# Performance work log

Hardware: AMD Instinct MI355X
Metric: run time of the kernel (lower is better)

## Reference

```python
import jax, jax.numpy as jnp
import numpy as np

D_MODEL = 512
NUM_HEADS = 4
KEY_DIM = 512          # expand_k = 1.0
VALUE_DIM = 1024       # expand_v = 2.0
HEAD_QK = KEY_DIM // NUM_HEADS    # 128
HEAD_V = VALUE_DIM // NUM_HEADS   # 256
GATE_LOW_RANK = 16
GATE_LOGIT_NORMALIZER = 16
EPS = 1e-5
CHUNK = 64
B, HH, WW = 8, 56, 56
N = HH * WW


def rmsnorm(x, w, eps=EPS):
    return x * jax.lax.rsqrt(jnp.mean(x * x, axis=-1, keepdims=True) + eps) * w


def gla_chunk(q, k, v, gk, scale, chunk=CHUNK):
    """Chunked gated linear attention (causal, decay gate on key dim).
    q,k,gk: [B,H,N,dk], v: [B,H,N,dv]. Recurrence:
      S_t = diag(exp(gk_t)) S_{t-1} + k_t^T v_t ;  o_t = (q_t*scale) S_t
    """
    Bb, Hh, Nn, dk = q.shape
    dv = v.shape[-1]
    nc = Nn // chunk

    def rc(t):  # [B,H,N,d] -> [nc,B,H,chunk,d]
        return jnp.moveaxis(t.reshape(Bb, Hh, nc, chunk, t.shape[-1]), 2, 0)

    qs, ks, vs, gs = rc(q), rc(k), rc(v), rc(gk)
    b = jnp.cumsum(gs, axis=-2)  # inclusive intra-chunk log-decay
    mask = jnp.tril(jnp.ones((chunk, chunk), bool))

    def step(S, inp):
        q_, k_, v_, b_ = inp
        qe = q_ * jnp.exp(b_) * scale                      # [B,H,C,dk]
        A = jnp.einsum('bhtd,bhsd->bhts', qe, k_ * jnp.exp(-b_))
        A = jnp.where(mask, A, 0.0)                        # causal intra-chunk
        o = jnp.einsum('bhts,bhsv->bhtv', A, v_) \
            + jnp.einsum('bhtd,bhdv->bhtv', qe, S)         # inter-chunk
        btot = b_[..., -1:, :]                             # [B,H,1,dk]
        S = S * jnp.exp(btot[..., 0, :])[..., None] \
            + jnp.einsum('bhtd,bhtv->bhdv', k_ * jnp.exp(btot - b_), v_)
        return S, o

    S0 = jnp.zeros((Bb, Hh, dk, dv), q.dtype)
    _, os = jax.lax.scan(step, S0, (qs, ks, vs, b))
    return jnp.moveaxis(os, 0, 2).reshape(Bb, Hh, Nn, dv)


def setup_inputs() -> dict:
    key = jax.random.key(0)
    ks = jax.random.split(key, 9)
    s = 0.02
    return {
        'x': jax.random.normal(ks[0], (B, N, D_MODEL), jnp.float32),
        'conv_w': jax.random.normal(ks[1], (D_MODEL, 1, 3, 3), jnp.float32) * s,
        'qkv_w': jax.random.normal(ks[2], (2 * KEY_DIM + VALUE_DIM, D_MODEL), jnp.float32) * s,
        'gk_w1': jax.random.normal(ks[3], (GATE_LOW_RANK, D_MODEL), jnp.float32) * s,
        'gk_w2': jax.random.normal(ks[4], (2 * KEY_DIM, GATE_LOW_RANK), jnp.float32) * s,
        'gk_b2': jax.random.normal(ks[5], (2 * KEY_DIM,), jnp.float32) * s,
        'g_w': jax.random.normal(ks[6], (VALUE_DIM, D_MODEL), jnp.float32) * s,
        'g_b': jax.random.normal(ks[7], (VALUE_DIM,), jnp.float32) * s,
        'gnorm_w': jnp.ones((HEAD_V,), jnp.float32),
        'lnorm_w': jnp.ones((HEAD_V,), jnp.float32),
        'o_w': jax.random.normal(ks[8], (D_MODEL, VALUE_DIM), jnp.float32) * s,
        'hw_h': HH,
        'hw_w': WW,
    }


def reference(x, conv_w, qkv_w, gk_w1, gk_w2, gk_b2, g_w, g_b,
              gnorm_w, lnorm_w, o_w, hw_h, hw_w):
    Bb, Nn, C = x.shape
    # in_proj: depthwise 3x3 conv over spatial layout + SiLU
    x2d = x.reshape(Bb, hw_h, hw_w, C).transpose(0, 3, 1, 2)
    x2d = jax.lax.conv_general_dilated(
        x2d, conv_w, (1, 1), 'SAME',
        dimension_numbers=('NCHW', 'OIHW', 'NCHW'), feature_group_count=C)
    xs = jax.nn.silu(x2d).transpose(0, 2, 3, 1).reshape(Bb, Nn, C)

    qkv = xs @ qkv_w.T
    q, k, v = jnp.split(qkv, [KEY_DIM, 2 * KEY_DIM], axis=-1)

    def heads(t, d):  # [B,N,h*d] -> [B,h,N,d]
        return t.reshape(Bb, Nn, NUM_HEADS, d).transpose(0, 2, 1, 3)

    q, k, v = heads(q, HEAD_QK), heads(k, HEAD_QK), heads(v, HEAD_V)

    # low-rank gate projection, two groups (forward / backward scan)
    gk = (xs @ gk_w1.T) @ gk_w2.T + gk_b2
    gk = jax.nn.log_sigmoid(gk) / GATE_LOGIT_NORMALIZER
    gk_f, gk_b = jnp.split(gk, 2, axis=-1)
    gk_f, gk_b = heads(gk_f, HEAD_QK), heads(gk_b, HEAD_QK)

    scale = HEAD_QK ** -0.5
    o_f = gla_chunk(q, k, v, gk_f, scale)
    flip = lambda t: t[:, :, ::-1]
    o_b = flip(gla_chunk(flip(q), flip(k), flip(v), flip(gk_b), scale))

    o = rmsnorm(o_f, gnorm_w) + rmsnorm(o_b, lnorm_w)   # [B,h,N,dv]
    o = o.transpose(0, 2, 1, 3).reshape(Bb, Nn, VALUE_DIM)
    g = xs @ g_w.T + g_b
    o = jax.nn.silu(g) * o                              # swish output gate
    return o @ o_w.T
```

## Files before the change

### kernel.cpp

```cpp
#include <hip/hip_runtime.h>
#include <hip/hip_bf16.h>
#include <math.h>

#define NHEADS 4
#define DMODEL 512
#define HQK 128
#define HV 256
#define BBATCH 8
#define SH 56
#define SWW 56
#define SEQN (SH*SWW)
#define NTOK (BBATCH*SEQN)
#define CH2 32
#define NC2 (SEQN/CH2)


typedef __bf16 bf16x8 __attribute__((ext_vector_type(8)));
typedef float  f32x4  __attribute__((ext_vector_type(4)));

__device__ __forceinline__ float silu_f(float v){ return v / (1.f + __expf(-v)); }

__device__ __forceinline__ float b2f(unsigned short u){
  union { unsigned int i; float f; } c; c.i = ((unsigned int)u) << 16; return c.f;
}
__device__ __forceinline__ unsigned short f2b(float f){
  __bf16 h = (__bf16)f;
  unsigned short u; __builtin_memcpy(&u, &h, 2); return u;
}
__device__ __forceinline__ float h2f(unsigned short u){
  _Float16 h; __builtin_memcpy(&h, &u, 2); return (float)h;
}
__device__ __forceinline__ unsigned short f2h(float f){
  _Float16 h = (_Float16)f; unsigned short u; __builtin_memcpy(&u, &h, 2); return u;
}
__device__ __forceinline__ float lsig16(float z){
  float e = __expf(-fabsf(z));
  return (fminf(z, 0.f) - __logf(1.f + e)) * 0.0625f;
}
__device__ __forceinline__ void up8(uint4 v, unsigned short* o){
  o[0]=(unsigned short)v.x; o[1]=(unsigned short)(v.x>>16);
  o[2]=(unsigned short)v.y; o[3]=(unsigned short)(v.y>>16);
  o[4]=(unsigned short)v.z; o[5]=(unsigned short)(v.z>>16);
  o[6]=(unsigned short)v.w; o[7]=(unsigned short)(v.w>>16);
}
__device__ __forceinline__ uint4 pk8(const unsigned short* s){
  uint4 v;
  v.x = (unsigned)s[0] | ((unsigned)s[1]<<16);
  v.y = (unsigned)s[2] | ((unsigned)s[3]<<16);
  v.z = (unsigned)s[4] | ((unsigned)s[5]<<16);
  v.w = (unsigned)s[6] | ((unsigned)s[7]<<16);
  return v;
}

#define GLL16(gp, lp) __builtin_amdgcn_global_load_lds( \
    (const __attribute__((address_space(1))) unsigned int*)(gp), \
    (__attribute__((address_space(3))) unsigned int*)(lp), 16, 0, 0)

__global__ __launch_bounds__(256) void k_w2b(const float* __restrict__ w,
                                             unsigned short* __restrict__ o, int n){
  int i = (blockIdx.x*256 + threadIdx.x) << 2;
  if (i >= n) return;
  float4 v = *(const float4*)&w[i];
  ushort4 p;
  p.x = f2b(v.x); p.y = f2b(v.y); p.z = f2b(v.z); p.w = f2b(v.w);
  *(ushort4*)&o[i] = p;
}

__global__ __launch_bounds__(256) void k_wc(const float* __restrict__ w1,
                                            const float* __restrict__ w2,
                                            unsigned short* __restrict__ wc){
  int idx = blockIdx.x*256 + threadIdx.x;
  int n = idx >> 9, k = idx & 511;
  float acc = 0.f;
  #pragma unroll
  for (int r=0;r<16;++r) acc += w2[n*16+r]*w1[r*512+k];
  wc[idx] = f2b(acc);
}

__global__ __launch_bounds__(256) void k_conv_silu(const float* __restrict__ x,
                                                   const float* __restrict__ cw,
                                                   unsigned short* __restrict__ xs){
  int gid = blockIdx.x*256 + threadIdx.x;
  int c4  = (gid & 127) << 2;
  int tok = gid >> 7;
  int b = tok / SEQN, sp = tok % SEQN;
  int hh = sp / SWW, ww = sp % SWW;
  float a0=0.f,a1=0.f,a2=0.f,a3=0.f;
  #pragma unroll
  for (int dh=-1; dh<=1; ++dh){
    int h2 = hh+dh; if (h2<0||h2>=SH) continue;
    #pragma unroll
    for (int dw=-1; dw<=1; ++dw){
      int w2 = ww+dw; if (w2<0||w2>=SWW) continue;
      const float4 xv = *(const float4*)&x[((size_t)(b*SEQN + h2*SWW + w2))*DMODEL + c4];
      int tap = (dh+1)*3 + (dw+1);
      a0 += xv.x * cw[(c4+0)*9 + tap];
      a1 += xv.y * cw[(c4+1)*9 + tap];
      a2 += xv.z * cw[(c4+2)*9 + tap];
      a3 += xv.w * cw[(c4+3)*9 + tap];
    }
  }
  ushort4 o;
  o.x = f2b(silu_f(a0)); o.y = f2b(silu_f(a1)); o.z = f2b(silu_f(a2)); o.w = f2b(silu_f(a3));
  *(ushort4*)&xs[(size_t)tok*DMODEL + c4] = o;
}

template<int ACT, int CBF>
__global__ __launch_bounds__(256) void k_gemm_mfma(const unsigned short* __restrict__ A,
                                                   const unsigned short* __restrict__ W,
                                                   const float* __restrict__ bias,
                                                   void* __restrict__ Cv,
                                                   int M, int N, int K){
  __shared__ unsigned short sA[128*32];
  __shared__ unsigned short sB[128*32];
  const int tid  = threadIdx.x;
  const int wave = tid >> 6, lane = tid & 63;
  const int lm = lane & 15, quad = lane >> 4;
  const int wm = wave & 1, wn = wave >> 1;
  const int nwg = gridDim.x * gridDim.y;
  const int hb  = blockIdx.y * gridDim.x + blockIdx.x;
  const int fb  = (hb & 7) * (nwg >> 3) + (hb >> 3);
  const int m0 = (fb / gridDim.x) * 128, n0 = (fb % gridDim.x) * 128;

  const int r0 = tid >> 2,  c0 = (tid & 3) << 3;
  const int f1 = tid + 256;
  const int r1 = f1 >> 2,   c1 = (f1 & 3) << 3;

  f32x4 acc[4][4] = {};

  for (int kt = 0; kt < K; kt += 32){
    GLL16(&A[(size_t)(m0 + r0)*K + kt + c0], &sA[(size_t)tid*8]);
    GLL16(&A[(size_t)(m0 + r1)*K + kt + c1], &sA[(size_t)f1*8]);
    GLL16(&W[(size_t)(n0 + r0)*K + kt + c0], &sB[(size_t)tid*8]);
    GLL16(&W[(size_t)(n0 + r1)*K + kt + c1], &sB[(size_t)f1*8]);
    __syncthreads();
    bf16x8 af[4], bf[4];
    #pragma unroll
    for (int i=0;i<4;++i) af[i] = *(const bf16x8*)&sA[(wm*64 + i*16 + lm)*32 + quad*8];
    #pragma unroll
    for (int j=0;j<4;++j) bf[j] = *(const bf16x8*)&sB[(wn*64 + j*16 + lm)*32 + quad*8];
    #pragma unroll
    for (int i=0;i<4;++i)
      #pragma unroll
      for (int j=0;j<4;++j)
        acc[i][j] = __builtin_amdgcn_mfma_f32_16x16x32_bf16(af[i], bf[j], acc[i][j], 0, 0, 0);
    __syncthreads();
  }

  #pragma unroll
  for (int i=0;i<4;++i){
    #pragma unroll
    for (int r=0;r<4;++r){
      size_t m = (size_t)(m0 + wm*64 + i*16 + quad*4 + r);
      #pragma unroll
      for (int j=0;j<4;++j){
        int n = n0 + wn*64 + j*16 + lm;
        float v = acc[i][j][r];
        if (bias) v += bias[n];
        if (ACT==1) v = silu_f(v);
        if (CBF) ((unsigned short*)Cv)[m*(size_t)N + n] = f2b(v);
        else     ((float*)Cv)[m*(size_t)N + n] = v;
      }
    }
  }
}

__global__ __launch_bounds__(256) void k_prep(unsigned short* __restrict__ qkv,
                                              const unsigned short* __restrict__ z,
                                              unsigned short* __restrict__ dbuf,
                                              unsigned short* __restrict__ ebF,
                                              unsigned short* __restrict__ ebB){
  const int blk = blockIdx.x;
  const int bb = blk / NC2, cB = blk % NC2;
  const int j  = threadIdx.x << 1;
  const int cb = j & 0x180;
  const int sl = j & 127;
  const int d1 = ((sl & 7) << 4) | (sl >> 3);
  const int d2 = d1 + 16;
  const size_t base = (size_t)bb*SEQN + cB*CH2;
  const float sc = 0.08838834764831845f;
  float bf0[CH2], bf1[CH2];
  float r0 = 0.f, r1 = 0.f;
  #pragma unroll
  for (int t=0;t<CH2;++t){
    size_t tok = base + t;
    float z0 = b2f(z[tok*1024 + cb + d1]);
    float z1 = b2f(z[tok*1024 + cb + d2]);
    r0 += lsig16(z0);
    r1 += lsig16(z1);
    bf0[t] = r0; bf1[t] = r1;
    float qv1 = b2f(qkv[tok*2048 + cb + d1]);
    float qv2 = b2f(qkv[tok*2048 + cb + d2]);
    float kv1 = b2f(qkv[tok*2048 + 512 + cb + d1]);
    float kv2 = b2f(qkv[tok*2048 + 512 + cb + d2]);
    float e0 = __expf(r0),  e1 = __expf(r1);
    float n0 = __expf(-r0), n1 = __expf(-r1);
    unsigned qo = (unsigned)f2b(qv1*e0*sc) | ((unsigned)f2b(qv2*e1*sc) << 16);
    unsigned ko = (unsigned)f2b(kv1*n0)    | ((unsigned)f2b(kv2*n1) << 16);
    __syncthreads();
    *(unsigned*)&qkv[tok*2048 + j] = qo;
    *(unsigned*)&qkv[tok*2048 + 512 + j] = ko;
  }
  const int hh = j >> 7;
  {
    int ef = ((bb*NHEADS + hh)*NC2 + cB)*HQK;
    ebF[ef + d1] = f2h(__expf(bf0[CH2-1]));
    ebF[ef + d2] = f2h(__expf(bf1[CH2-1]));
  }
  r0 = 0.f; r1 = 0.f;
  #pragma unroll
  for (int t=CH2-1;t>=0;--t){
    size_t tok = base + t;
    float z0 = b2f(z[tok*1024 + 512 + cb + d1]);
    float z1 = b2f(z[tok*1024 + 512 + cb + d2]);
    r0 += lsig16(z0);
    r1 += lsig16(z1);
    float dd0 = r0 - bf0[t], dd1 = r1 - bf1[t];
    *(unsigned*)&dbuf[tok*512 + j] = (unsigned)f2h(__expf(dd0))
                                   | ((unsigned)f2h(__expf(dd1)) << 16);
  }
  {
    int eb = ((bb*NHEADS + hh)*NC2 + (NC2-1-cB))*HQK;
    ebB[eb + d1] = f2h(__expf(r0));
    ebB[eb + d2] = f2h(__expf(r1));
  }
}

#define SKET_STORE(sKeT_, kb_, o8_, ts_) \
  _Pragma("unroll") \
  for (int u=0;u<8;++u){ \
    (sKeT_)[(u*16 + 2*(o8_)    )*40 + (ts_)] = (kb_)[u]; \
    (sKeT_)[(u*16 + 2*(o8_) + 1)*40 + (ts_)] = (kb_)[u+8]; \
  }

__global__ __launch_bounds__(256,3) void k_gla_state(const unsigned short* __restrict__ qkvb,
                                                     const unsigned short* __restrict__ dbuf,
                                                     const unsigned short* __restrict__ ebFt,
                                                     const unsigned short* __restrict__ ebBt,
                                                     float* __restrict__ dSseg){
  __shared__ __align__(16) unsigned short sKeT[2][128*40];
  __shared__ __align__(16) unsigned short sVT[2][128*40];
  __shared__ float sEb[2][128];

  const int tid = threadIdx.x;
  const int bx = blockIdx.x;
  const int combo = bx & 127, seg = bx >> 7;
  const int vp = combo & 1, dir = (combo>>1)&1, hh = (combo>>2)&3, bb = (combo>>4)&7;

  const int w = tid >> 6, lane = tid & 63;
  const int quad = lane >> 4, lm = lane & 15;
  const int ts = tid >> 3, o8 = tid & 7, d16 = o8 << 4;
  const int tl = tid & 31, vg = tid >> 5;

  const int kcol = 512 + hh*HQK, vcol = 1024 + hh*HV + vp*128;
  const int dcol = hh*HQK;
  const unsigned short* ebT = dir ? ebBt : ebFt;
  const int ebBase = (bb*NHEADS + hh)*NC2*HQK;
  const int c0 = (seg==0)?0:(seg==1)?13:(seg==2)?25:(seg==3)?37:(seg==4)?50:62;
  const int c1 = (seg==0)?13:(seg==1)?25:(seg==2)?37:(seg==3)?50:(seg==4)?62:74;

#define STSTAGE(c_, bi_) { \
    int p_ = (c_)*CH2 + ts; \
    int n_ = dir ? (SEQN-1-p_) : p_; \
    size_t tok_ = (size_t)bb*SEQN + n_; \
    uint4 k0_ = *(const uint4*)&qkvb[tok_*2048 + kcol + d16]; \
    uint4 k1_ = *(const uint4*)&qkvb[tok_*2048 + kcol + d16 + 8]; \
    unsigned short kb_[16]; \
    up8(k0_, kb_); up8(k1_, kb_+8); \
    if (dir){ \
      uint4 dd0_ = *(const uint4*)&dbuf[tok_*512 + dcol + d16]; \
      uint4 dd1_ = *(const uint4*)&dbuf[tok_*512 + dcol + d16 + 8]; \
      unsigned short eh_[16]; \
      up8(dd0_, eh_); up8(dd1_, eh_+8); \
      _Pragma("unroll") \
      for (int u=0;u<16;++u) \
        kb_[u] = f2b(b2f(kb_[u]) * __builtin_amdgcn_rcpf(h2f(eh_[u]))); \
    } \
    SKET_STORE(sKeT[bi_], kb_, o8, ts); \
    int pv_ = (c_)*CH2 + tl; \
    int nv_ = dir ? (SEQN-1-pv_) : pv_; \
    size_t tokv_ = (size_t)bb*SEQN + nv_; \
    uint4 uv0_ = *(const uint4*)&qkvb[tokv_*2048 + vcol + vg*8]; \
    uint4 uv1_ = *(const uint4*)&qkvb[tokv_*2048 + vcol + 64 + vg*8]; \
    unsigned short su_[8]; \
    up8(uv0_, su_); \
    _Pragma("unroll") \
    for (int u=0;u<8;++u) sVT[bi_][(vg*8+u)*40 + tl] = su_[u]; \
    up8(uv1_, su_); \
    _Pragma("unroll") \
    for (int u=0;u<8;++u) sVT[bi_][(64+vg*8+u)*40 + tl] = su_[u]; \
    if (tid < 128) sEb[bi_][tid] = h2f(ebT[ebBase + (c_)*HQK + tid]); \
  }

  f32x4 Sreg[2][8];
  #pragma unroll
  for (int vh=0; vh<2; ++vh)
    #pragma unroll
    for (int i=0;i<8;++i)
      #pragma unroll
      for (int r=0;r<4;++r) Sreg[vh][i][r] = 0.f;

  STSTAGE(c0, 0);
  __syncthreads();
  for (int c = c0; c < c1; ++c){
    const int cur = (c - c0) & 1;
    if (c + 1 < c1) STSTAGE(c+1, cur^1);
    bf16x8 vta0 = *(const bf16x8*)&sVT[cur][(w*16+lm)*40 + quad*8];
    bf16x8 vta1 = *(const bf16x8*)&sVT[cur][(64 + w*16+lm)*40 + quad*8];
    #pragma unroll
    for (int dt=0; dt<8; ++dt){
      bf16x8 kt = *(const bf16x8*)&sKeT[cur][(dt*16+lm)*40 + quad*8];
      float eb = sEb[cur][dt*16 + lm];
      Sreg[0][dt] = __builtin_amdgcn_mfma_f32_16x16x32_bf16(vta0, kt, Sreg[0][dt], 0, 0, 0);
      Sreg[1][dt] = __builtin_amdgcn_mfma_f32_16x16x32_bf16(vta1, kt, Sreg[1][dt], 0, 0, 0);
      #pragma unroll
      for (int r=0;r<4;++r){ Sreg[0][dt][r] *= eb; Sreg[1][dt][r] *= eb; }
    }
    __syncthreads();
  }
#undef STSTAGE

  #pragma unroll
  for (int vh=0; vh<2; ++vh){
    const int combo_s = (vp*2+vh) | (dir<<2) | (hh<<3) | (bb<<5);
    const size_t sbase = ((size_t)seg*256 + combo_s) * 8192;
    #pragma unroll
    for (int dt=0; dt<8; ++dt){
      #pragma unroll
      for (int r=0;r<4;++r)
        dSseg[sbase + (size_t)(w*16 + quad*4 + r)*128 + dt*16 + lm] = Sreg[vh][dt][r];
    }
  }
}

__global__ __launch_bounds__(256) void k_gla_comb(const float* __restrict__ dSseg,
                                                  float* __restrict__ dSf,
                                                  const unsigned short* __restrict__ ebFt,
                                                  const unsigned short* __restrict__ ebBt){
  const int combo = blockIdx.x;
  const int dir = (combo>>2)&1, hh = (combo>>3)&3, bb = (combo>>5)&7;
  const unsigned short* ebT = dir ? ebBt : ebFt;
  const int ebBase = (bb*NHEADS + hh)*NC2*HQK;
  const int t = threadIdx.x;
  const int d0 = (t << 2) & 127;
  float D1[4]={1,1,1,1}, D2[4]={1,1,1,1}, D3[4]={1,1,1,1}, D4[4]={1,1,1,1}, D5[4]={1,1,1,1};
  for (int c=13; c<25; ++c){
    ushort4 ev = *(const ushort4*)&ebT[ebBase + c*HQK + d0];
    D1[0]*=h2f(ev.x); D1[1]*=h2f(ev.y); D1[2]*=h2f(ev.z); D1[3]*=h2f(ev.w);
  }
  for (int c=25; c<37; ++c){
    ushort4 ev = *(const ushort4*)&ebT[ebBase + c*HQK + d0];
    D2[0]*=h2f(ev.x); D2[1]*=h2f(ev.y); D2[2]*=h2f(ev.z); D2[3]*=h2f(ev.w);
  }
  for (int c=37; c<50; ++c){
    ushort4 ev = *(const ushort4*)&ebT[ebBase + c*HQK + d0];
    D3[0]*=h2f(ev.x); D3[1]*=h2f(ev.y); D3[2]*=h2f(ev.z); D3[3]*=h2f(ev.w);
  }
  for (int c=50; c<62; ++c){
    ushort4 ev = *(const ushort4*)&ebT[ebBase + c*HQK + d0];
    D4[0]*=h2f(ev.x); D4[1]*=h2f(ev.y); D4[2]*=h2f(ev.z); D4[3]*=h2f(ev.w);
  }
  for (int c=62; c<74; ++c){
    ushort4 ev = *(const ushort4*)&ebT[ebBase + c*HQK + d0];
    D5[0]*=h2f(ev.x); D5[1]*=h2f(ev.y); D5[2]*=h2f(ev.z); D5[3]*=h2f(ev.w);
  }
  const size_t bA = (size_t)combo*8192;
  const size_t SEG = (size_t)256*8192;
  #pragma unroll
  for (int r=0;r<8;++r){
    int idx = r*1024 + (t<<2);
    float4 a0 = *(const float4*)&dSseg[bA + idx];
    float4 a1 = *(const float4*)&dSseg[bA + SEG + idx];
    float4 a2 = *(const float4*)&dSseg[bA + 2*SEG + idx];
    float4 a3 = *(const float4*)&dSseg[bA + 3*SEG + idx];
    float4 a4 = *(const float4*)&dSseg[bA + 4*SEG + idx];
    float4 a5 = *(const float4*)&dSseg[bA + 5*SEG + idx];
    float4 s25, s50, s74;
    s25.x = D1[0]*a0.x + a1.x; s25.y = D1[1]*a0.y + a1.y;
    s25.z = D1[2]*a0.z + a1.z; s25.w = D1[3]*a0.w + a1.w;
    s50.x = D3[0]*(D2[0]*s25.x + a2.x) + a3.x;
    s50.y = D3[1]*(D2[1]*s25.y + a2.y) + a3.y;
    s50.z = D3[2]*(D2[2]*s25.z + a2.z) + a3.z;
    s50.w = D3[3]*(D2[3]*s25.w + a2.w) + a3.w;
    s74.x = D5[0]*(D4[0]*s50.x + a4.x) + a5.x;
    s74.y = D5[1]*(D4[1]*s50.y + a4.y) + a5.y;
    s74.z = D5[2]*(D4[2]*s50.z + a4.z) + a5.z;
    s74.w = D5[3]*(D4[3]*s50.w + a4.w) + a5.w;
    *(float4*)&dSf[bA + idx] = s25;
    *(float4*)&dSf[SEG + bA + idx] = s50;
    *(float4*)&dSf[2*SEG + bA + idx] = s74;
  }
}

__global__ __launch_bounds__(256,2) void k_gla3(const unsigned short* __restrict__ qkvb,
                                                const unsigned short* __restrict__ dbuf,
                                                const unsigned short* __restrict__ ebFt,
                                                const unsigned short* __restrict__ ebBt,
                                                unsigned short* __restrict__ og,
                                                const float* __restrict__ dSf){
  __shared__ __align__(16) unsigned short sQe[32*136];
  __shared__ __align__(16) unsigned short sKe[32*136];
  __shared__ __align__(16) unsigned short sKeT[128*40];
  __shared__ __align__(16) unsigned short sVT[128*40];
  __shared__ __align__(16) unsigned short sST[128*136];
  __shared__ __align__(16) unsigned short sP[32*40];
  __shared__ float sEb[128];

  const int tid = threadIdx.x;
  const int bx = blockIdx.x;
  const int combo = bx & 127, seg = bx >> 7;
  const int vp = combo & 1, dir = (combo>>1)&1, hh = (combo>>2)&3, bb = (combo>>4)&7;

  const int w = tid >> 6, lane = tid & 63;
  const int quad = lane >> 4, lm = lane & 15;
  const int mt = w >> 1, nt = w & 1;
  const int ts = tid >> 3, o8 = tid & 7, d16 = o8 << 4;
  const int tl = tid & 31, vg = tid >> 5;

  const int qcol = hh*HQK, kcol = 512 + hh*HQK, vcol = 1024 + hh*HV + vp*128;
  const int dcol = hh*HQK;
  const unsigned short* ebT = dir ? ebBt : ebFt;
  const int ebBase = (bb*NHEADS + hh)*NC2*HQK;
  const size_t ogBase = ((size_t)((dir*BBATCH + bb)*NHEADS + hh)) * SEQN * HV;

  f32x4 Sreg[2][8];
  #pragma unroll
  for (int vh=0; vh<2; ++vh)
    #pragma unroll
    for (int i=0;i<8;++i)
      #pragma unroll
      for (int r=0;r<4;++r) Sreg[vh][i][r] = 0.f;
  if (seg){
    #pragma unroll
    for (int vh=0; vh<2; ++vh){
      const int combo_s = (vp*2+vh) | (dir<<2) | (hh<<3) | (bb<<5);
      const size_t sbase = ((size_t)(seg-1)*256 + combo_s) * 8192;
      #pragma unroll
      for (int dt=0; dt<8; ++dt){
        #pragma unroll
        for (int r=0;r<4;++r){
          float sv = dSf[sbase + (size_t)(w*16 + quad*4 + r)*128 + dt*16 + lm];
          Sreg[vh][dt][r] = sv;
          sST[(vh*64 + w*16 + quad*4 + r)*136 + lm*8 + dt] = f2b(sv);
        }
      }
    }
  } else {
    for (int i = tid; i < 128*136; i += 256) sST[i] = 0;
  }
  __syncthreads();

  const int cBeg = (seg==0)?0:(seg==1)?25:(seg==2)?50:74;
  const int cEnd = (seg==0)?25:(seg==1)?50:(seg==2)?74:98;

  for (int c = cBeg; c < cEnd; ++c){
    {
      int p = c*CH2 + ts;
      int n = dir ? (SEQN-1-p) : p;
      size_t tok = (size_t)bb*SEQN + n;
      uint4 q0 = *(const uint4*)&qkvb[tok*2048 + qcol + d16];
      uint4 q1 = *(const uint4*)&qkvb[tok*2048 + qcol + d16 + 8];
      uint4 k0 = *(const uint4*)&qkvb[tok*2048 + kcol + d16];
      uint4 k1 = *(const uint4*)&qkvb[tok*2048 + kcol + d16 + 8];
      unsigned short kb[16];
      up8(k0, kb); up8(k1, kb+8);
      if (dir){
        uint4 dd0 = *(const uint4*)&dbuf[tok*512 + dcol + d16];
        uint4 dd1 = *(const uint4*)&dbuf[tok*512 + dcol + d16 + 8];
        unsigned short eh[16], qb[16];
        up8(dd0, eh); up8(dd1, eh+8);
        up8(q0, qb);  up8(q1, qb+8);
        #pragma unroll
        for (int u=0;u<16;++u){
          float e  = h2f(eh[u]);
          float ei = __builtin_amdgcn_rcpf(e);
          qb[u] = f2b(b2f(qb[u]) * e);
          kb[u] = f2b(b2f(kb[u]) * ei);
        }
        q0 = pk8(qb); q1 = pk8(qb+8);
        k0 = pk8(kb); k1 = pk8(kb+8);
      }
      *(uint4*)&sQe[ts*136 + d16]     = q0;
      *(uint4*)&sQe[ts*136 + d16 + 8] = q1;
      *(uint4*)&sKe[ts*136 + d16]     = k0;
      *(uint4*)&sKe[ts*136 + d16 + 8] = k1;
      SKET_STORE(sKeT, kb, o8, ts);
      int pv = c*CH2 + tl;
      int nv = dir ? (SEQN-1-pv) : pv;
      size_t tokv = (size_t)bb*SEQN + nv;
      uint4 uv0 = *(const uint4*)&qkvb[tokv*2048 + vcol + vg*8];
      uint4 uv1 = *(const uint4*)&qkvb[tokv*2048 + vcol + 64 + vg*8];
      unsigned short su[8];
      up8(uv0, su);
      #pragma unroll
      for (int u=0;u<8;++u) sVT[(vg*8+u)*40 + tl] = su[u];
      up8(uv1, su);
      #pragma unroll
      for (int u=0;u<8;++u) sVT[(64+vg*8+u)*40 + tl] = su[u];
    }
    if (tid < 128) sEb[tid] = h2f(ebT[ebBase + c*HQK + tid]);
    __syncthreads();
    bf16x8 qf[2][4];
    #pragma unroll
    for (int tt=0; tt<2; ++tt){
      #pragma unroll
      for (int ks=0; ks<4; ++ks)
        qf[tt][ks] = *(const bf16x8*)&sQe[(tt*16+lm)*136 + ks*32 + quad*8];
    }
    f32x4 a1;
    #pragma unroll
    for (int r=0;r<4;++r) a1[r] = 0.f;
    #pragma unroll
    for (int ks=0; ks<4; ++ks){
      bf16x8 kfr = *(const bf16x8*)&sKe[(nt*16+lm)*136 + ks*32 + quad*8];
      a1 = __builtin_amdgcn_mfma_f32_16x16x32_bf16(qf[mt][ks], kfr, a1, 0, 0, 0);
    }
    f32x4 ot[2][2];
    #pragma unroll
    for (int vh=0; vh<2; ++vh)
      #pragma unroll
      for (int tt=0; tt<2; ++tt)
        #pragma unroll
        for (int r=0;r<4;++r) ot[vh][tt][r] = 0.f;
    #pragma unroll
    for (int ks=0; ks<4; ++ks){
      #pragma unroll
      for (int vh=0; vh<2; ++vh){
        bf16x8 stf = *(const bf16x8*)&sST[(vh*64 + w*16+lm)*136 + ks*32 + quad*8];
        #pragma unroll
        for (int tt=0; tt<2; ++tt)
          ot[vh][tt] = __builtin_amdgcn_mfma_f32_16x16x32_bf16(stf, qf[tt][ks], ot[vh][tt], 0, 0, 0);
      }
    }
    #pragma unroll
    for (int r=0;r<4;++r){
      int t = mt*16 + quad*4 + r, s = nt*16 + lm;
      sP[t*40 + s] = f2b((s <= t) ? a1[r] : 0.f);
    }
    __syncthreads();
    bf16x8 vta[2];
    vta[0] = *(const bf16x8*)&sVT[(w*16+lm)*40 + quad*8];
    vta[1] = *(const bf16x8*)&sVT[(64 + w*16+lm)*40 + quad*8];
    #pragma unroll
    for (int dt=0; dt<8; ++dt){
      bf16x8 kt = *(const bf16x8*)&sKeT[(dt*16+lm)*40 + quad*8];
      float eb = sEb[dt*16 + lm];
      #pragma unroll
      for (int vh=0; vh<2; ++vh){
        Sreg[vh][dt] = __builtin_amdgcn_mfma_f32_16x16x32_bf16(vta[vh], kt, Sreg[vh][dt], 0, 0, 0);
        #pragma unroll
        for (int r=0;r<4;++r) Sreg[vh][dt][r] *= eb;
      }
    }
    #pragma unroll
    for (int vh=0; vh<2; ++vh){
      #pragma unroll
      for (int r=0;r<4;++r){
        uint4 pkv;
        pkv.x = (unsigned)f2b(Sreg[vh][0][r]) | ((unsigned)f2b(Sreg[vh][1][r]) << 16);
        pkv.y = (unsigned)f2b(Sreg[vh][2][r]) | ((unsigned)f2b(Sreg[vh][3][r]) << 16);
        pkv.z = (unsigned)f2b(Sreg[vh][4][r]) | ((unsigned)f2b(Sreg[vh][5][r]) << 16);
        pkv.w = (unsigned)f2b(Sreg[vh][6][r]) | ((unsigned)f2b(Sreg[vh][7][r]) << 16);
        *(uint4*)&sST[(vh*64 + w*16 + quad*4 + r)*136 + lm*8] = pkv;
      }
    }
    #pragma unroll
    for (int tt=0; tt<2; ++tt){
      bf16x8 pf = *(const bf16x8*)&sP[(tt*16+lm)*40 + quad*8];
      int p = c*CH2 + tt*16 + lm;
      int n = dir ? (SEQN-1-p) : p;
      #pragma unroll
      for (int vh=0; vh<2; ++vh){
        ot[vh][tt] = __builtin_amdgcn_mfma_f32_16x16x32_bf16(vta[vh], pf, ot[vh][tt], 0, 0, 0);
        ushort4 o4;
        o4.x = f2b(ot[vh][tt][0]); o4.y = f2b(ot[vh][tt][1]);
        o4.z = f2b(ot[vh][tt][2]); o4.w = f2b(ot[vh][tt][3]);
        *(ushort4*)&og[ogBase + (size_t)n*HV + vp*128 + vh*64 + w*16 + quad*4] = o4;
      }
    }
    __syncthreads();
  }
}

__global__ __launch_bounds__(256) void k_gate(const unsigned short* __restrict__ og,
                                              const unsigned short* __restrict__ g,
                                              const float* __restrict__ gnw,
                                              const float* __restrict__ lnw,
                                              unsigned short* __restrict__ y){
  int tok = blockIdx.x;
  int bb = tok / SEQN, n = tok % SEQN;
  int hh = threadIdx.x >> 6, l = threadIdx.x & 63;
  int j4 = l << 2;
  size_t basef = ((size_t)((0*BBATCH+bb)*NHEADS+hh))*SEQN*HV + (size_t)n*HV + j4;
  size_t baseb = ((size_t)((1*BBATCH+bb)*NHEADS+hh))*SEQN*HV + (size_t)n*HV + j4;
  ushort4 ofu = *(const ushort4*)&og[basef];
  ushort4 obu = *(const ushort4*)&og[baseb];
  float of0=b2f(ofu.x), of1=b2f(ofu.y), of2=b2f(ofu.z), of3=b2f(ofu.w);
  float ob0=b2f(obu.x), ob1=b2f(obu.y), ob2=b2f(obu.z), ob3=b2f(obu.w);
  float ssf = of0*of0 + of1*of1 + of2*of2 + of3*of3;
  float ssb = ob0*ob0 + ob1*ob1 + ob2*ob2 + ob3*ob3;
  #pragma unroll
  for (int m=32;m>=1;m>>=1){ ssf += __shfl_xor(ssf,m,64); ssb += __shfl_xor(ssb,m,64); }
  float rf = rsqrtf(ssf*(1.f/HV) + 1e-5f);
  float rb = rsqrtf(ssb*(1.f/HV) + 1e-5f);
  float4 gn = *(const float4*)&gnw[j4];
  float4 ln = *(const float4*)&lnw[j4];
  ushort4 gvu = *(const ushort4*)&g[(size_t)tok*1024 + hh*HV + j4];
  float g0=b2f(gvu.x), g1=b2f(gvu.y), g2=b2f(gvu.z), g3=b2f(gvu.w);
  ushort4 out;
  out.x = f2b(g0*(of0*rf*gn.x + ob0*rb*ln.x));
  out.y = f2b(g1*(of1*rf*gn.y + ob1*rb*ln.y));
  out.z = f2b(g2*(of2*rf*gn.z + ob2*rb*ln.z));
  out.w = f2b(g3*(of3*rf*gn.w + ob3*rb*ln.w));
  *(ushort4*)&y[(size_t)tok*1024 + hh*HV + j4] = out;
}

extern "C" void kernel_launch(void* const* d_in, const int* in_sizes, int n_in,
                              void* d_out, int out_size, void* d_ws, size_t ws_size,
                              hipStream_t stream){
  (void)in_sizes; (void)n_in; (void)out_size;
  const float* x    = (const float*)d_in[0];
  const float* cw   = (const float*)d_in[1];
  const float* qkvw = (const float*)d_in[2];
  const float* gkw1 = (const float*)d_in[3];
  const float* gkw2 = (const float*)d_in[4];
  const float* gkb2 = (const float*)d_in[5];
  const float* gw   = (const float*)d_in[6];
  const float* gb   = (const float*)d_in[7];
  const float* gnw  = (const float*)d_in[8];
  const float* lnw  = (const float*)d_in[9];
  const float* ow   = (const float*)d_in[10];

  if (ws_size < 232816640u) return;
  char* wsb = (char*)d_ws;
  char* dob = (char*)d_out;
  unsigned short* qkv  = (unsigned short*)(wsb + 0);
  unsigned short* g    = (unsigned short*)(wsb + 51380224);
  unsigned short* og   = (unsigned short*)(wsb + 102760448);
  float*          dSseg= (float*)(wsb + 102760448);
  unsigned short* zbuf = (unsigned short*)(wsb + 102760448 + 25690112);
  unsigned short* wqb  = (unsigned short*)(wsb + 102760448 + 77070336);
  unsigned short* wc   = (unsigned short*)(wsb + 102760448 + 80216064);
  unsigned short* dbuf = (unsigned short*)(wsb + 205520896);
  unsigned short* wgb  = (unsigned short*)(wsb + 205520896);
  unsigned short* ebF  = (unsigned short*)(wsb + 231211008);
  unsigned short* ebB  = (unsigned short*)(wsb + 232013824);
  unsigned short* xs   = (unsigned short*)(dob + 0);
  float*          dSf  = (float*)(dob + 25690112);
  unsigned short* wob  = og;
  unsigned short* y    = qkv;
  float*          outp = (float*)d_out;

  k_conv_silu<<<NTOK*128/256, 256, 0, stream>>>(x, cw, xs);
  k_w2b<<<1024, 256, 0, stream>>>(qkvw, wqb, 2048*512);
  k_wc<<<2048, 256, 0, stream>>>(gkw1, gkw2, wc);
  k_gemm_mfma<0,1><<<dim3(16,196), 256, 0, stream>>>(xs, wqb, nullptr, qkv,  NTOK, 2048, 512);
  k_gemm_mfma<0,1><<<dim3(8,196),  256, 0, stream>>>(xs, wc,  gkb2,    zbuf, NTOK, 1024, 512);
  k_prep<<<BBATCH*NC2, 256, 0, stream>>>(qkv, zbuf, dbuf, ebF, ebB);
  k_gla_state<<<768, 256, 0, stream>>>(qkv, dbuf, ebF, ebB, dSseg);
  k_gla_comb<<<256, 256, 0, stream>>>(dSseg, dSf, ebF, ebB);
  k_gla3<<<512, 256, 0, stream>>>(qkv, dbuf, ebF, ebB, og, dSf);
  k_w2b<<<512,  256, 0, stream>>>(gw, wgb, 1024*512);
  k_gemm_mfma<1,1><<<dim3(8,196),  256, 0, stream>>>(xs, wgb, gb, g, NTOK, 1024, 512);
  k_gate<<<NTOK, 256, 0, stream>>>(og, g, gnw, lnw, y);
  k_w2b<<<512, 256, 0, stream>>>(ow, wob, 512*1024);
  k_gemm_mfma<0,0><<<dim3(4,196), 256, 0, stream>>>(y, wob, nullptr, outp, NTOK, 512, 1024);
}
```

Baseline: 1.084 ms.

## Double-buffer K/V staging and load Q/K MFMA fragments directly from global

In the GLA chunk kernel, the K-transpose, V-transpose and decay tiles are now double-buffered in shared memory. The next chunk's global loads are issued at the top of the iteration and written to the alternate buffer at the end, which removes one barrier per chunk and overlaps load latency with the MFMA work. The Q and K fragments for the intra-chunk attention are read straight from global into registers, with the decay scaling applied inline, so the sQe/sKe shared tiles go away. In exchange, some global traffic is redundant across waves, the backward direction does more per-element decay math, and register pressure rises under launch_bounds(256,2).

Result: slower. 1.188 ms (+9.6%).

```diff
diff --git a/kernel.cpp b/kernel.cpp
--- a/kernel.cpp
+++ b/kernel.cpp
@@ -50,6 +50,9 @@
   v.z = (unsigned)s[4] | ((unsigned)s[5]<<16);
   v.w = (unsigned)s[6] | ((unsigned)s[7]<<16);
   return v;
+}
+__device__ __forceinline__ bf16x8 u2b8(uint4 v){
+  bf16x8 r; __builtin_memcpy(&r, &v, 16); return r;
 }
 
 #define GLL16(gp, lp) __builtin_amdgcn_global_load_lds( \
@@ -398,13 +401,11 @@
                                                 const unsigned short* __restrict__ ebBt,
                                                 unsigned short* __restrict__ og,
                                                 const float* __restrict__ dSf){
-  __shared__ __align__(16) unsigned short sQe[32*136];
-  __shared__ __align__(16) unsigned short sKe[32*136];
-  __shared__ __align__(16) unsigned short sKeT[128*40];
-  __shared__ __align__(16) unsigned short sVT[128*40];
+  __shared__ __align__(16) unsigned short sKeT[2][128*40];
+  __shared__ __align__(16) unsigned short sVT[2][128*40];
   __shared__ __align__(16) unsigned short sST[128*136];
   __shared__ __align__(16) unsigned short sP[32*40];
-  __shared__ float sEb[128];
+  __shared__ float sEb[2][128];
 
   const int tid = threadIdx.x;
   const int bx = blockIdx.x;
@@ -422,6 +423,46 @@
   const unsigned short* ebT = dir ? ebBt : ebFt;
   const int ebBase = (bb*NHEADS + hh)*NC2*HQK;
   const size_t ogBase = ((size_t)((dir*BBATCH + bb)*NHEADS + hh)) * SEQN * HV;
+
+  uint4 pk0, pk1, pd0, pd1, pv0, pv1;
+
+#define STLOAD(c_) { \
+    int p_ = (c_)*CH2 + ts; \
+    int n_ = dir ? (SEQN-1-p_) : p_; \
+    size_t tok_ = (size_t)bb*SEQN + n_; \
+    pk0 = *(const uint4*)&qkvb[tok_*2048 + kcol + d16]; \
+    pk1 = *(const uint4*)&qkvb[tok_*2048 + kcol + d16 + 8]; \
+    if (dir){ \
+      pd0 = *(const uint4*)&dbuf[tok_*512 + dcol + d16]; \
+      pd1 = *(const uint4*)&dbuf[tok_*512 + dcol + d16 + 8]; \
+    } \
+    int pv_ = (c_)*CH2 + tl; \
+    int nv_ = dir ? (SEQN-1-pv_) : pv_; \
+    size_t tokv_ = (size_t)bb*SEQN + nv_; \
+    pv0 = *(const uint4*)&qkvb[tokv_*2048 + vcol + vg*8]; \
+    pv1 = *(const uint4*)&qkvb[tokv_*2048 + vcol + 64 + vg*8]; \
+  }
+
+#define STWRITE(bi_, c_) { \
+    unsigned short kb_[16]; \
+    up8(pk0, kb_); up8(pk1, kb_+8); \
+    if (dir){ \
+      unsigned short eh_[16]; \
+      up8(pd0, eh_); up8(pd1, eh_+8); \
+      _Pragma("unroll") \
+      for (int u=0;u<16;++u) \
+        kb_[u] = f2b(b2f(kb_[u]) * __builtin_amdgcn_rcpf(h2f(eh_[u]))); \
+    } \
+    SKET_STORE(sKeT[bi_], kb_, o8, ts); \
+    unsigned short su_[8]; \
+    up8(pv0, su_); \
+    _Pragma("unroll") \
+    for (int u=0;u<8;++u) sVT[bi_][(vg*8+u)*40 + tl] = su_[u]; \
+    up8(pv1, su_); \
+    _Pragma("unroll") \
+    for (int u=0;u<8;++u) sVT[bi_][(64+vg*8+u)*40 + tl] = su_[u]; \
+    if (tid < 128) sEb[bi_][tid] = h2f(ebT[ebBase + (c_)*HQK + tid]); \
+  }
 
   f32x4 Sreg[2][8];
   #pragma unroll
@@ -448,72 +489,61 @@
   } else {
     for (int i = tid; i < 128*136; i += 256) sST[i] = 0;
   }
-  __syncthreads();
 
   const int cBeg = (seg==0)?0:(seg==1)?25:(seg==2)?50:74;
   const int cEnd = (seg==0)?25:(seg==1)?50:(seg==2)?74:98;
 
+  STLOAD(cBeg);
+  STWRITE(0, cBeg);
+  __syncthreads();
+
   for (int c = cBeg; c < cEnd; ++c){
+    const int cur = (c - cBeg) & 1;
+    const bool hn = (c + 1 < cEnd);
+    if (hn) STLOAD(c+1);
+    bf16x8 qf[2][4];
+    #pragma unroll
+    for (int tt=0; tt<2; ++tt){
+      int pq = c*CH2 + tt*16 + lm;
+      int nq = dir ? (SEQN-1-pq) : pq;
+      const unsigned short* qrow = &qkvb[((size_t)bb*SEQN + nq)*2048 + qcol];
+      const unsigned short* erow = &dbuf[((size_t)bb*SEQN + nq)*512 + dcol];
+      #pragma unroll
+      for (int ks=0; ks<4; ++ks){
+        uint4 qv = *(const uint4*)&qrow[ks*32 + quad*8];
+        if (dir){
+          uint4 ev = *(const uint4*)&erow[ks*32 + quad*8];
+          unsigned short qb[8], e8[8];
+          up8(qv, qb); up8(ev, e8);
+          #pragma unroll
+          for (int u=0;u<8;++u) qb[u] = f2b(b2f(qb[u]) * h2f(e8[u]));
+          qv = pk8(qb);
+        }
+        qf[tt][ks] = u2b8(qv);
+      }
+    }
+    f32x4 a1;
+    #pragma unroll
+    for (int r=0;r<4;++r) a1[r] = 0.f;
     {
-      int p = c*CH2 + ts;
-      int n = dir ? (SEQN-1-p) : p;
-      size_t tok = (size_t)bb*SEQN + n;
-      uint4 q0 = *(const uint4*)&qkvb[tok*2048 + qcol + d16];
-      uint4 q1 = *(const uint4*)&qkvb[tok*2048 + qcol + d16 + 8];
-      uint4 k0 = *(const uint4*)&qkvb[tok*2048 + kcol + d16];
-      uint4 k1 = *(const uint4*)&qkvb[tok*2048 + kcol + d16 + 8];
-      unsigned short kb[16];
-      up8(k0, kb); up8(k1, kb+8);
-      if (dir){
-        uint4 dd0 = *(const uint4*)&dbuf[tok*512 + dcol + d16];
-        uint4 dd1 = *(const uint4*)&dbuf[tok*512 + dcol + d16 + 8];
-        unsigned short eh[16], qb[16];
-        up8(dd0, eh); up8(dd1, eh+8);
-        up8(q0, qb);  up8(q1, qb+8);
-        #pragma unroll
-        for (int u=0;u<16;++u){
-          float e  = h2f(eh[u]);
-          float ei = __builtin_amdgcn_rcpf(e);
-          qb[u] = f2b(b2f(qb[u]) * e);
-          kb[u] = f2b(b2f(kb[u]) * ei);
+      int pk_ = c*CH2 + nt*16 + lm;
+      int nk = dir ? (SEQN-1-pk_) : pk_;
+      const unsigned short* krow = &qkvb[((size_t)bb*SEQN + nk)*2048 + kcol];
+      const unsigned short* erow = &dbuf[((size_t)bb*SEQN + nk)*512 + dcol];
+      #pragma unroll
+      for (int ks=0; ks<4; ++ks){
+        uint4 kv = *(const uint4*)&krow[ks*32 + quad*8];
+        if (dir){
+          uint4 ev = *(const uint4*)&erow[ks*32 + quad*8];
+          unsigned short kb2[8], e8[8];
+          up8(kv, kb2); up8(ev, e8);
+          #pragma unroll
+          for (int u=0;u<8;++u)
+            kb2[u] = f2b(b2f(kb2[u]) * __builtin_amdgcn_rcpf(h2f(e8[u])));
+          kv = pk8(kb2);
         }
-        q0 = pk8(qb); q1 = pk8(qb+8);
-        k0 = pk8(kb); k1 = pk8(kb+8);
+        a1 = __builtin_amdgcn_mfma_f32_16x16x32_bf16(qf[mt][ks], u2b8(kv), a1, 0, 0, 0);
       }
-      *(uint4*)&sQe[ts*136 + d16]     = q0;
-      *(uint4*)&sQe[ts*136 + d16 + 8] = q1;
-      *(uint4*)&sKe[ts*136 + d16]     = k0;
-      *(uint4*)&sKe[ts*136 + d16 + 8] = k1;
-      SKET_STORE(sKeT, kb, o8, ts);
-      int pv = c*CH2 + tl;
-      int nv = dir ? (SEQN-1-pv) : pv;
-      size_t tokv = (size_t)bb*SEQN + nv;
-      uint4 uv0 = *(const uint4*)&qkvb[tokv*2048 + vcol + vg*8];
-      uint4 uv1 = *(const uint4*)&qkvb[tokv*2048 + vcol + 64 + vg*8];
-      unsigned short su[8];
-      up8(uv0, su);
-      #pragma unroll
-      for (int u=0;u<8;++u) sVT[(vg*8+u)*40 + tl] = su[u];
-      up8(uv1, su);
-      #pragma unroll
-      for (int u=0;u<8;++u) sVT[(64+vg*8+u)*40 + tl] = su[u];
-    }
-    if (tid < 128) sEb[tid] = h2f(ebT[ebBase + c*HQK + tid]);
-    __syncthreads();
-    bf16x8 qf[2][4];
-    #pragma unroll
-    for (int tt=0; tt<2; ++tt){
-      #pragma unroll
-      for (int ks=0; ks<4; ++ks)
-        qf[tt][ks] = *(const bf16x8*)&sQe[(tt*16+lm)*136 + ks*32 + quad*8];
-    }
-    f32x4 a1;
-    #pragma unroll
-    for (int r=0;r<4;++r) a1[r] = 0.f;
-    #pragma unroll
-    for (int ks=0; ks<4; ++ks){
-      bf16x8 kfr = *(const bf16x8*)&sKe[(nt*16+lm)*136 + ks*32 + quad*8];
-      a1 = __builtin_amdgcn_mfma_f32_16x16x32_bf16(qf[mt][ks], kfr, a1, 0, 0, 0);
     }
     f32x4 ot[2][2];
     #pragma unroll
@@ -539,12 +569,12 @@
     }
     __syncthreads();
     bf16x8 vta[2];
-    vta[0] = *(const bf16x8*)&sVT[(w*16+lm)*40 + quad*8];
-    vta[1] = *(const bf16x8*)&sVT[(64 + w*16+lm)*40 + quad*8];
+    vta[0] = *(const bf16x8*)&sVT[cur][(w*16+lm)*40 + quad*8];
+    vta[1] = *(const bf16x8*)&sVT[cur][(64 + w*16+lm)*40 + quad*8];
     #pragma unroll
     for (int dt=0; dt<8; ++dt){
-      bf16x8 kt = *(const bf16x8*)&sKeT[(dt*16+lm)*40 + quad*8];
-      float eb = sEb[dt*16 + lm];
+      bf16x8 kt = *(const bf16x8*)&sKeT[cur][(dt*16+lm)*40 + quad*8];
+      float eb = sEb[cur][dt*16 + lm];
       #pragma unroll
       for (int vh=0; vh<2; ++vh){
         Sreg[vh][dt] = __builtin_amdgcn_mfma_f32_16x16x32_bf16(vta[vh], kt, Sreg[vh][dt], 0, 0, 0);
@@ -578,8 +608,11 @@
         *(ushort4*)&og[ogBase + (size_t)n*HV + vp*128 + vh*64 + w*16 + quad*4] = o4;
       }
     }
+    if (hn) STWRITE(cur^1, c+1);
     __syncthreads();
   }
+#undef STLOAD
+#undef STWRITE
 }
 
 __global__ __launch_bounds__(256) void k_gate(const unsigned short* __restrict__ og,
```
